# Kernel tuning notes

Measured on AMD Instinct MI355X. Metric: run time of the kernel, lower is better.

The kernel has to match this reference:

```python
import jax, jax.numpy as jnp
import numpy as np

N_HEAD = 16
N_FEAT = 1024
D_K = N_FEAT // N_HEAD
B, S = 2, 2048


def setup_inputs() -> dict:
    key = jax.random.key(0)
    ks = jax.random.split(key, 13)
    s = 1.0 / np.sqrt(N_FEAT)
    return {
        "query": jax.random.normal(ks[0], (B, S, N_FEAT), jnp.float32),
        "key": jax.random.normal(ks[1], (B, S, N_FEAT), jnp.float32),
        "value": jax.random.normal(ks[2], (B, S, N_FEAT), jnp.float32),
        "mask": jax.random.randint(ks[3], (B, 1, S), 0, 2).astype(bool),
        "w_q": jax.random.uniform(ks[4], (N_FEAT, N_FEAT), jnp.float32, -s, s),
        "b_q": jax.random.uniform(ks[5], (N_FEAT,), jnp.float32, -s, s),
        "w_k": jax.random.uniform(ks[6], (N_FEAT, N_FEAT), jnp.float32, -s, s),
        "b_k": jax.random.uniform(ks[7], (N_FEAT,), jnp.float32, -s, s),
        "w_v": jax.random.uniform(ks[8], (N_FEAT, N_FEAT), jnp.float32, -s, s),
        "b_v": jax.random.uniform(ks[9], (N_FEAT,), jnp.float32, -s, s),
        "w_o": jax.random.uniform(ks[10], (N_FEAT, N_FEAT), jnp.float32, -s, s),
        "b_o": jax.random.uniform(ks[11], (N_FEAT,), jnp.float32, -s, s),
    }


def reference(query, key, value, mask, w_q, b_q, w_k, b_k, w_v, b_v, w_o, b_o):
    b = query.shape[0]
    # projections -> [b, h, s, d_k]
    def proj(x, w, bias):
        y = x @ w.T + bias
        return y.reshape(b, -1, N_HEAD, D_K).transpose(0, 2, 1, 3)

    q = proj(query, w_q, b_q)
    k = proj(key, w_k, b_k)
    v = proj(value, w_v, b_v)

    scores = jnp.einsum("bhqd,bhkd->bhqk", q, k) / jnp.sqrt(jnp.asarray(D_K, q.dtype))
    m = mask[:, None]  # [b,1,1,s] broadcast over heads and query positions
    scores = jnp.where(m, jnp.asarray(-10000.0, scores.dtype), scores)
    attn = jax.nn.softmax(scores, axis=-1)
    attn = jnp.where(m, jnp.asarray(0.0, attn.dtype), attn)
    x = jnp.einsum("bhqk,bhkd->bhqd", attn, v)
    x = x.transpose(0, 2, 1, 3).reshape(b, -1, N_HEAD * D_K)
    return x @ w_o.T + b_o
```

## Files before the change

kernel.cpp:

```cpp
#include <hip/hip_runtime.h>
#include <hip/hip_bf16.h>


typedef float f32x4 __attribute__((ext_vector_type(4)));
typedef short bf16x8 __attribute__((ext_vector_type(8)));
typedef short bf16x4 __attribute__((ext_vector_type(4)));

typedef const __attribute__((address_space(1))) void* gas_ptr;
typedef __attribute__((address_space(3))) void* las_ptr;

#if __has_builtin(__builtin_amdgcn_exp2f)
#define EXP2(x) __builtin_amdgcn_exp2f(x)
#else
#define EXP2(x) exp2f(x)
#endif
#define LOG2E 1.4426950408889634f

static __device__ __forceinline__ short to_bf16s(float f) {
    __hip_bfloat16 h = __float2bfloat16(f);
    return __builtin_bit_cast(short, h);
}
static __device__ __forceinline__ unsigned pack_bf16(float a, float b) {
    unsigned lo = (unsigned short)__builtin_bit_cast(short, __float2bfloat16(a));
    unsigned hi = (unsigned short)__builtin_bit_cast(short, __float2bfloat16(b));
    return lo | (hi << 16);
}
static __device__ __forceinline__ bf16x4 pack4(float a, float b, float c, float d) {
    unsigned long long u = (unsigned long long)pack_bf16(a, b)
                         | ((unsigned long long)pack_bf16(c, d) << 32);
    return __builtin_bit_cast(bf16x4, u);
}
static __device__ __forceinline__ f32x4 mfma16(bf16x4 a, bf16x4 b, f32x4 c) {
#if __has_builtin(__builtin_amdgcn_mfma_f32_16x16x16bf16_1k)
    return __builtin_amdgcn_mfma_f32_16x16x16bf16_1k(a, b, c, 0, 0, 0);
#else
    asm("v_mfma_f32_16x16x16_bf16 %0, %1, %2, %0" : "+v"(c) : "v"(a), "v"(b));
    return c;
#endif
}

__global__ void cvt3_kernel(const float* __restrict__ s0, const float* __restrict__ s1,
                            const float* __restrict__ s2, short* __restrict__ d0,
                            short* __restrict__ d1, short* __restrict__ d2) {
    const int g = blockIdx.x;
    const int sel = g >> 12;
    const int i = (g & 4095) * 256 + threadIdx.x;
    const float* s = sel == 0 ? s0 : (sel == 1 ? s1 : s2);
    short* d = sel == 0 ? d0 : (sel == 1 ? d1 : d2);
    float4 v = reinterpret_cast<const float4*>(s)[i];
    short4 o;
    o.x = to_bf16s(v.x); o.y = to_bf16s(v.y); o.z = to_bf16s(v.z); o.w = to_bf16s(v.w);
    reinterpret_cast<short4*>(d)[i] = o;
}
__global__ void cvt4_kernel(const float* __restrict__ s0, const float* __restrict__ s1,
                            const float* __restrict__ s2, const float* __restrict__ s3,
                            short* __restrict__ d0, short* __restrict__ d1,
                            short* __restrict__ d2, short* __restrict__ d3) {
    const int g = blockIdx.x;
    const int sel = g >> 10;
    const int i = (g & 1023) * 256 + threadIdx.x;
    const float* s = sel == 0 ? s0 : (sel == 1 ? s1 : (sel == 2 ? s2 : s3));
    short* d = sel == 0 ? d0 : (sel == 1 ? d1 : (sel == 2 ? d2 : d3));
    float4 v = reinterpret_cast<const float4*>(s)[i];
    short4 o;
    o.x = to_bf16s(v.x); o.y = to_bf16s(v.y); o.z = to_bf16s(v.z); o.w = to_bf16s(v.w);
    reinterpret_cast<short4*>(d)[i] = o;
}

__global__ void maskf_kernel(const int* __restrict__ mask, float* __restrict__ mf) {
    int i = blockIdx.x * 256 + threadIdx.x;
    mf[i] = mask[i] ? (-10000.0f * LOG2E) : 0.0f;
}


static __device__ __forceinline__ void stage_tile(
    short* sa, short* sb, const short* A, const short* W,
    int m0, int n0, int k0, int tid)
{
#pragma unroll
    for (int rnd = 0; rnd < 2; ++rnd) {
        const int t = rnd * 256 + tid;
        const int c2 = t & 7;
        const int row = 2 * (t >> 3) + (c2 & 1);
        const int col = (c2 >> 1) * 8;
        __builtin_amdgcn_global_load_lds((gas_ptr)(A + (long)(m0 + row) * 1024 + k0 + col),
                                         (las_ptr)(sa + t * 8), 16, 0, 0);
        __builtin_amdgcn_global_load_lds((gas_ptr)(W + (long)(n0 + row) * 1024 + k0 + col),
                                         (las_ptr)(sb + t * 8), 16, 0, 0);
    }
}

static __device__ __forceinline__ void gemm_compute(
    const short* sa, const short* sb, int wr, int wc, int aoff, f32x4 (&acc)[4][4])
{
    bf16x8 af[4], bfr[4];
#pragma unroll
    for (int i = 0; i < 4; ++i)
        af[i] = *reinterpret_cast<const bf16x8*>(sa + (wr + i * 16) * 32 + aoff);
#pragma unroll
    for (int j = 0; j < 4; ++j)
        bfr[j] = *reinterpret_cast<const bf16x8*>(sb + (wc + j * 16) * 32 + aoff);
#pragma unroll
    for (int i = 0; i < 4; ++i)
#pragma unroll
        for (int j = 0; j < 4; ++j)
            acc[i][j] = __builtin_amdgcn_mfma_f32_16x16x32_bf16(af[i], bfr[j], acc[i][j], 0, 0, 0);
}

__global__ __launch_bounds__(256, 3) void proj_gemm(
    const short* __restrict__ A0, const short* __restrict__ A1, const short* __restrict__ A2,
    const short* __restrict__ W0, const short* __restrict__ W1, const short* __restrict__ W2,
    const float* __restrict__ bi0, const float* __restrict__ bi1, const float* __restrict__ bi2,
    short* __restrict__ o0, short* __restrict__ o1, short* __restrict__ o2)
{
    __shared__ __align__(16) short sa[2][4096];
    __shared__ __align__(16) short sb[2][4096];
    const int z = blockIdx.z;
    const short* A = z == 0 ? A0 : (z == 1 ? A1 : A2);
    const short* W = z == 0 ? W0 : (z == 1 ? W1 : W2);
    const float* bias = z == 0 ? bi0 : (z == 1 ? bi1 : bi2);
    short* outp = z == 0 ? o0 : (z == 1 ? o1 : o2);

    const int tid = threadIdx.x;
    const int w = tid >> 6, l = tid & 63;
    const int lr = l & 15, lh = l >> 4;
    const int m0 = blockIdx.x * 128, n0 = blockIdx.y * 128;
    const int wr = (w >> 1) * 64, wc = (w & 1) * 64;
    const int aoff = (lr >> 1) * 64 + (lr & 1) * 8 + lh * 16;

    f32x4 acc[4][4] = {};

    stage_tile(sa[0], sb[0], A, W, m0, n0, 0, tid);
    __syncthreads();
    for (int k0 = 0; k0 < 1024; k0 += 64) {
        stage_tile(sa[1], sb[1], A, W, m0, n0, k0 + 32, tid);
        gemm_compute(sa[0], sb[0], wr, wc, aoff, acc);
        __syncthreads();
        if (k0 + 64 < 1024)
            stage_tile(sa[0], sb[0], A, W, m0, n0, k0 + 64, tid);
        gemm_compute(sa[1], sb[1], wr, wc, aoff, acc);
        __syncthreads();
    }

    const float scl = (z == 0) ? 0.125f * LOG2E : 1.0f;
#pragma unroll
    for (int i = 0; i < 4; ++i) {
#pragma unroll
        for (int j = 0; j < 4; ++j) {
#pragma unroll
            for (int r = 0; r < 4; ++r) {
                const int row = m0 + wr + i * 16 + lh * 4 + r;
                const int col = n0 + wc + j * 16 + lr;
                const float v = (acc[i][j][r] + bias[col]) * scl;
                const int b = row >> 11, s = row & 2047;
                const int h = col >> 6, d = col & 63;
                if (z != 2)
                    outp[(((long)(b * 16 + h)) * 2048 + s) * 64 + d] = to_bf16s(v);
                else
                    outp[(((long)(b * 16 + h)) * 64 + d) * 2048 + s] = to_bf16s(v);
            }
        }
    }
}

__global__ __launch_bounds__(256, 2) void out_gemm(
    const short* __restrict__ A, const short* __restrict__ W,
    const float* __restrict__ bias, float* __restrict__ outp)
{
    __shared__ __align__(16) short sa[2][4096];
    __shared__ __align__(16) short sb[2][4096];
    const int tid = threadIdx.x;
    const int w = tid >> 6, l = tid & 63;
    const int lr = l & 15, lh = l >> 4;
    const int m0 = blockIdx.x * 128, n0 = blockIdx.y * 128;
    const int wr = (w >> 1) * 64, wc = (w & 1) * 64;
    const int aoff = (lr >> 1) * 64 + (lr & 1) * 8 + lh * 16;

    f32x4 acc[4][4] = {};

    stage_tile(sa[0], sb[0], A, W, m0, n0, 0, tid);
    __syncthreads();
    for (int k0 = 0; k0 < 1024; k0 += 64) {
        stage_tile(sa[1], sb[1], A, W, m0, n0, k0 + 32, tid);
        gemm_compute(sa[0], sb[0], wr, wc, aoff, acc);
        __syncthreads();
        if (k0 + 64 < 1024)
            stage_tile(sa[0], sb[0], A, W, m0, n0, k0 + 64, tid);
        gemm_compute(sa[1], sb[1], wr, wc, aoff, acc);
        __syncthreads();
    }

#pragma unroll
    for (int i = 0; i < 4; ++i)
#pragma unroll
        for (int j = 0; j < 4; ++j)
#pragma unroll
            for (int r = 0; r < 4; ++r) {
                const int row = m0 + wr + i * 16 + lh * 4 + r;
                const int col = n0 + wc + j * 16 + lr;
                outp[(long)row * 1024 + col] = acc[i][j][r] + bias[col];
            }
}


static __device__ __forceinline__ void stage_kv(
    short* ldsKb, short* ldsVb, const short* Kg, const short* Vg,
    int key0, int w, int srow, int schunk)
{
    __builtin_amdgcn_global_load_lds((gas_ptr)(Kg + (long)(key0 + srow) * 64 + schunk * 8),
                                     (las_ptr)(ldsKb + w * 512), 16, 0, 0);
    __builtin_amdgcn_global_load_lds((gas_ptr)(Kg + (long)(key0 + srow + 32) * 64 + schunk * 8),
                                     (las_ptr)(ldsKb + 2048 + w * 512), 16, 0, 0);
    __builtin_amdgcn_global_load_lds((gas_ptr)(Vg + (long)srow * 2048 + key0 + schunk * 8),
                                     (las_ptr)(ldsVb + w * 512), 16, 0, 0);
    __builtin_amdgcn_global_load_lds((gas_ptr)(Vg + (long)(srow + 32) * 2048 + key0 + schunk * 8),
                                     (las_ptr)(ldsVb + 2048 + w * 512), 16, 0, 0);
}

static __device__ __forceinline__ void attn_step(
    const short* __restrict__ Kbuf, const short* __restrict__ Vbuf,
    const float* __restrict__ ldsM, int key0,
    const bf16x8 (&qf)[2][2], int lr, int lh, int sw,
    float (&mreg)[2], float (&lsum)[2], f32x4 (&ao)[2][4])
{
    f32x4 mb[4];
#pragma unroll
    for (int s = 0; s < 4; ++s)
        mb[s] = *reinterpret_cast<const f32x4*>(ldsM + key0 + s * 16 + lh * 4);

    f32x4 sc[2][4];
#pragma unroll
    for (int s = 0; s < 4; ++s) {
        const short* kb = Kbuf + (s * 16 + lr) * 64;
        bf16x8 k0 = *reinterpret_cast<const bf16x8*>(kb + (((lh * 16) ^ sw) >> 1));
        bf16x8 k1 = *reinterpret_cast<const bf16x8*>(kb + (((64 + lh * 16) ^ sw) >> 1));
        f32x4 z = {};
        sc[0][s] = __builtin_amdgcn_mfma_f32_16x16x32_bf16(k0, qf[0][0], z, 0, 0, 0);
        sc[0][s] = __builtin_amdgcn_mfma_f32_16x16x32_bf16(k1, qf[0][1], sc[0][s], 0, 0, 0);
        sc[1][s] = __builtin_amdgcn_mfma_f32_16x16x32_bf16(k0, qf[1][0], z, 0, 0, 0);
        sc[1][s] = __builtin_amdgcn_mfma_f32_16x16x32_bf16(k1, qf[1][1], sc[1][s], 0, 0, 0);
    }

    bf16x4 pb[2][4];
#pragma unroll
    for (int j = 0; j < 2; ++j) {
        float t = -1e30f;
#pragma unroll
        for (int s = 0; s < 4; ++s)
#pragma unroll
            for (int r = 0; r < 4; ++r) {
                const float v = sc[j][s][r] + mb[s][r];
                sc[j][s][r] = v;
                t = fmaxf(t, v);
            }
        t = fmaxf(t, __shfl_xor(t, 16));
        t = fmaxf(t, __shfl_xor(t, 32));
        if (__any(t > mreg[j] + 8.0f)) {
            const float mn = fmaxf(mreg[j], t);
            const float sf = EXP2(mreg[j] - mn);
            lsum[j] *= sf;
#pragma unroll
            for (int d4 = 0; d4 < 4; ++d4) ao[j][d4] *= sf;
            mreg[j] = mn;
        }
        float ps = 0.f;
#pragma unroll
        for (int s = 0; s < 4; ++s) {
            const float p0 = EXP2(sc[j][s][0] - mreg[j]);
            const float p1 = EXP2(sc[j][s][1] - mreg[j]);
            const float p2 = EXP2(sc[j][s][2] - mreg[j]);
            const float p3 = EXP2(sc[j][s][3] - mreg[j]);
            ps += (p0 + p1) + (p2 + p3);
            pb[j][s] = pack4(p0, p1, p2, p3);
        }
        ps += __shfl_xor(ps, 16);
        ps += __shfl_xor(ps, 32);
        lsum[j] += ps;
    }

#pragma unroll
    for (int s = 0; s < 4; ++s) {
#pragma unroll
        for (int d4 = 0; d4 < 4; ++d4) {
            const short* vb = Vbuf + (d4 * 16 + lr) * 64;
            bf16x4 vf = *reinterpret_cast<const bf16x4*>(vb + (((s * 32 + lh * 8) ^ sw) >> 1));
            ao[0][d4] = mfma16(vf, pb[0][s], ao[0][d4]);
            ao[1][d4] = mfma16(vf, pb[1][s], ao[1][d4]);
        }
    }
}

__global__ __launch_bounds__(256, 2) void attn_kernel(
    const short* __restrict__ Q, const short* __restrict__ Kmat,
    const short* __restrict__ Vt, const float* __restrict__ maskf,
    short* __restrict__ X)
{
    __shared__ __align__(16) short ldsK[2][4096];
    __shared__ __align__(16) short ldsV[2][4096];
    __shared__ __align__(16) float ldsM[2048];

    const int id = blockIdx.x;
    const int slot = id >> 3;
    const int bh = (id & 7) * 4 + (slot >> 4);
    const int q0 = (slot & 15) * 128;
    const int b = bh >> 4, h = bh & 15;
    const int w = threadIdx.x >> 6, l = threadIdx.x & 63;
    const int lr = l & 15, lh = l >> 4;
    const int sw = (lr & 7) << 4;

    const int srow = w * 8 + (l >> 3);
    const int schunk = (l & 7) ^ (srow & 7);

    const short* Kg = Kmat + (long)bh * 2048 * 64;
    const short* Vg = Vt + (long)bh * 64 * 2048;

#pragma unroll
    for (int rnd = 0; rnd < 2; ++rnd) {
        const int t = rnd * 256 + threadIdx.x;
        __builtin_amdgcn_global_load_lds((gas_ptr)(maskf + (long)b * 2048 + t * 4),
                                         (las_ptr)(ldsM + t * 4), 16, 0, 0);
    }

    const short* Qp = Q + ((long)bh * 2048 + q0 + w * 32 + lr) * 64 + lh * 8;
    bf16x8 qf[2][2];
    qf[0][0] = *reinterpret_cast<const bf16x8*>(Qp);
    qf[0][1] = *reinterpret_cast<const bf16x8*>(Qp + 32);
    qf[1][0] = *reinterpret_cast<const bf16x8*>(Qp + 16 * 64);
    qf[1][1] = *reinterpret_cast<const bf16x8*>(Qp + 16 * 64 + 32);

    float mreg[2] = {-1e30f, -1e30f}, lsum[2] = {0.f, 0.f};
    f32x4 ao[2][4] = {};

    stage_kv(ldsK[0], ldsV[0], Kg, Vg, 0, w, srow, schunk);
    __syncthreads();

    for (int tt = 0; tt < 16; ++tt) {
        const int key0 = tt * 128;
        stage_kv(ldsK[1], ldsV[1], Kg, Vg, key0 + 64, w, srow, schunk);
        attn_step(ldsK[0], ldsV[0], ldsM, key0, qf, lr, lh, sw, mreg, lsum, ao);
        __syncthreads();
        if (tt < 15)
            stage_kv(ldsK[0], ldsV[0], Kg, Vg, key0 + 128, w, srow, schunk);
        attn_step(ldsK[1], ldsV[1], ldsM, key0 + 64, qf, lr, lh, sw, mreg, lsum, ao);
        __syncthreads();
    }

#pragma unroll
    for (int j = 0; j < 2; ++j) {
        const float inv = 1.0f / fmaxf(lsum[j], 1e-30f);
        const int s = q0 + w * 32 + j * 16 + lr;
        short* Xp = X + ((long)b * 2048 + s) * 1024 + h * 64 + lh * 4;
#pragma unroll
        for (int d4 = 0; d4 < 4; ++d4) {
            short4 o;
            o.x = to_bf16s(ao[j][d4][0] * inv);
            o.y = to_bf16s(ao[j][d4][1] * inv);
            o.z = to_bf16s(ao[j][d4][2] * inv);
            o.w = to_bf16s(ao[j][d4][3] * inv);
            *reinterpret_cast<short4*>(Xp + d4 * 16) = o;
        }
    }
}

extern "C" void kernel_launch(void* const* d_in, const int* in_sizes, int n_in,
                              void* d_out, int out_size, void* d_ws, size_t ws_size,
                              hipStream_t stream) {
    const float* query = (const float*)d_in[0];
    const float* key_  = (const float*)d_in[1];
    const float* value = (const float*)d_in[2];
    const int*   mask  = (const int*)d_in[3];
    const float* w_q = (const float*)d_in[4];
    const float* b_q = (const float*)d_in[5];
    const float* w_k = (const float*)d_in[6];
    const float* b_k = (const float*)d_in[7];
    const float* w_v = (const float*)d_in[8];
    const float* b_v = (const float*)d_in[9];
    const float* w_o = (const float*)d_in[10];
    const float* b_o = (const float*)d_in[11];

    const long SEQ = 4194304;
    const long WSZ = 1048576;
    short* ws = (short*)d_ws;
    short* cq = ws;
    short* ck = cq + SEQ;
    short* cv = ck + SEQ;
    short* wq = cv + SEQ;
    short* wk = wq + WSZ;
    short* wv = wk + WSZ;
    short* wo = wv + WSZ;
    short* Qb = wo + WSZ;
    short* Kb = Qb + SEQ;
    short* Vt = Kb + SEQ;
    short* Xb = cq;
    float* mkf = (float*)cv;

    cvt3_kernel<<<12288, 256, 0, stream>>>(query, key_, value, cq, ck, cv);
    cvt4_kernel<<<4096, 256, 0, stream>>>(w_q, w_k, w_v, w_o, wq, wk, wv, wo);

    dim3 blk(256);
    proj_gemm<<<dim3(32, 8, 3), blk, 0, stream>>>(cq, ck, cv, wq, wk, wv,
                                                  b_q, b_k, b_v, Qb, Kb, Vt);

    maskf_kernel<<<16, 256, 0, stream>>>(mask, mkf);

    attn_kernel<<<512, blk, 0, stream>>>(Qb, Kb, Vt, mkf, Xb);

    out_gemm<<<dim3(32, 8), blk, 0, stream>>>(Xb, wo, b_o, (float*)d_out);
}
```

Baseline: 148.0 us.

## Use 16x16x32 MFMA for PV via key permutation, shrink out_gemm N tile

The attention PV product switches from 16x16x16 to 16x16x32 MFMAs. K rows and mask entries are permuted so the score accumulator layout matches the B-operand layout the wider instruction expects, which halves the number of PV MFMAs. The mask bias is folded into the QK MFMA accumulator init instead of a separate add. Separately, out_gemm uses 128x64 tiles with twice as many blocks to improve occupancy and CU fill, at the cost of more A-tile reloads.

```diff
diff --git a/kernel.cpp b/kernel.cpp
--- a/kernel.cpp
+++ b/kernel.cpp
@@ -4,7 +4,6 @@
 
 typedef float f32x4 __attribute__((ext_vector_type(4)));
 typedef short bf16x8 __attribute__((ext_vector_type(8)));
-typedef short bf16x4 __attribute__((ext_vector_type(4)));
 
 typedef const __attribute__((address_space(1))) void* gas_ptr;
 typedef __attribute__((address_space(3))) void* las_ptr;
@@ -25,18 +24,13 @@
     unsigned hi = (unsigned short)__builtin_bit_cast(short, __float2bfloat16(b));
     return lo | (hi << 16);
 }
-static __device__ __forceinline__ bf16x4 pack4(float a, float b, float c, float d) {
-    unsigned long long u = (unsigned long long)pack_bf16(a, b)
-                         | ((unsigned long long)pack_bf16(c, d) << 32);
-    return __builtin_bit_cast(bf16x4, u);
-}
-static __device__ __forceinline__ f32x4 mfma16(bf16x4 a, bf16x4 b, f32x4 c) {
-#if __has_builtin(__builtin_amdgcn_mfma_f32_16x16x16bf16_1k)
-    return __builtin_amdgcn_mfma_f32_16x16x16bf16_1k(a, b, c, 0, 0, 0);
-#else
-    asm("v_mfma_f32_16x16x16_bf16 %0, %1, %2, %0" : "+v"(c) : "v"(a), "v"(b));
-    return c;
-#endif
+static __device__ __forceinline__ bf16x8 pack8(const float* p) {
+    unsigned d0 = pack_bf16(p[0], p[1]);
+    unsigned d1 = pack_bf16(p[2], p[3]);
+    unsigned d2 = pack_bf16(p[4], p[5]);
+    unsigned d3 = pack_bf16(p[6], p[7]);
+    unsigned u4[4] = {d0, d1, d2, d3};
+    return __builtin_bit_cast(bf16x8, u4);
 }
 
 __global__ void cvt3_kernel(const float* __restrict__ s0, const float* __restrict__ s1,
@@ -68,10 +62,11 @@
 }
 
 __global__ void maskf_kernel(const int* __restrict__ mask, float* __restrict__ mf) {
-    int i = blockIdx.x * 256 + threadIdx.x;
-    mf[i] = mask[i] ? (-10000.0f * LOG2E) : 0.0f;
-}
-
+    const int i = blockIdx.x * 256 + threadIdx.x;
+    const int p = i & 31;
+    const int phi = 8 * ((p >> 2) & 3) + 4 * (p >> 4) + (p & 3);
+    mf[i] = mask[(i & ~31) | phi] ? (-10000.0f * LOG2E) : 0.0f;
+}
 
 static __device__ __forceinline__ void stage_tile(
     short* sa, short* sb, const short* A, const short* W,
@@ -168,32 +163,64 @@
     const float* __restrict__ bias, float* __restrict__ outp)
 {
     __shared__ __align__(16) short sa[2][4096];
-    __shared__ __align__(16) short sb[2][4096];
+    __shared__ __align__(16) short sb[2][2048];
     const int tid = threadIdx.x;
     const int w = tid >> 6, l = tid & 63;
     const int lr = l & 15, lh = l >> 4;
-    const int m0 = blockIdx.x * 128, n0 = blockIdx.y * 128;
-    const int wr = (w >> 1) * 64, wc = (w & 1) * 64;
+    const int m0 = blockIdx.x * 128, n0 = blockIdx.y * 64;
+    const int wr = (w >> 1) * 64, wc = (w & 1) * 32;
     const int aoff = (lr >> 1) * 64 + (lr & 1) * 8 + lh * 16;
 
-    f32x4 acc[4][4] = {};
-
-    stage_tile(sa[0], sb[0], A, W, m0, n0, 0, tid);
+    f32x4 acc[4][2] = {};
+
+    const int c2 = tid & 7;
+    const int brow = 2 * (tid >> 3) + (c2 & 1);
+    const int bcol = (c2 >> 1) * 8;
+
+    auto stage = [&](short* pa, short* pb, int k0) {
+#pragma unroll
+        for (int rnd = 0; rnd < 2; ++rnd) {
+            const int t = rnd * 256 + tid;
+            const int cc = t & 7;
+            const int row = 2 * (t >> 3) + (cc & 1);
+            const int col = (cc >> 1) * 8;
+            __builtin_amdgcn_global_load_lds((gas_ptr)(A + (long)(m0 + row) * 1024 + k0 + col),
+                                             (las_ptr)(pa + t * 8), 16, 0, 0);
+        }
+        __builtin_amdgcn_global_load_lds((gas_ptr)(W + (long)(n0 + brow) * 1024 + k0 + bcol),
+                                         (las_ptr)(pb + tid * 8), 16, 0, 0);
+    };
+    auto compute = [&](const short* pa, const short* pb) {
+        bf16x8 af[4], bfr[2];
+#pragma unroll
+        for (int i = 0; i < 4; ++i)
+            af[i] = *reinterpret_cast<const bf16x8*>(pa + (wr + i * 16) * 32 + aoff);
+#pragma unroll
+        for (int j = 0; j < 2; ++j)
+            bfr[j] = *reinterpret_cast<const bf16x8*>(pb + (wc + j * 16) * 32 + aoff);
+#pragma unroll
+        for (int i = 0; i < 4; ++i)
+#pragma unroll
+            for (int j = 0; j < 2; ++j)
+                acc[i][j] = __builtin_amdgcn_mfma_f32_16x16x32_bf16(af[i], bfr[j], acc[i][j], 0, 0, 0);
+    };
+
+    stage(sa[0], sb[0], 0);
     __syncthreads();
     for (int k0 = 0; k0 < 1024; k0 += 64) {
-        stage_tile(sa[1], sb[1], A, W, m0, n0, k0 + 32, tid);
-        gemm_compute(sa[0], sb[0], wr, wc, aoff, acc);
+        stage(sa[1], sb[1], k0 + 32);
+        compute(sa[0], sb[0]);
         __syncthreads();
         if (k0 + 64 < 1024)
-            stage_tile(sa[0], sb[0], A, W, m0, n0, k0 + 64, tid);
-        gemm_compute(sa[1], sb[1], wr, wc, aoff, acc);
+            stage(sa[0], sb[0], k0 + 64);
+        compute(sa[1], sb[1]);
         __syncthreads();
     }
 
 #pragma unroll
     for (int i = 0; i < 4; ++i)
 #pragma unroll
-        for (int j = 0; j < 4; ++j)
+        for (int j = 0; j < 2; ++j)
 #pragma unroll
             for (int r = 0; r < 4; ++r) {
                 const int row = m0 + wr + i * 16 + lh * 4 + r;
@@ -205,11 +232,11 @@
 
 static __device__ __forceinline__ void stage_kv(
     short* ldsKb, short* ldsVb, const short* Kg, const short* Vg,
-    int key0, int w, int srow, int schunk)
-{
-    __builtin_amdgcn_global_load_lds((gas_ptr)(Kg + (long)(key0 + srow) * 64 + schunk * 8),
+    int key0, int w, int srow, int prow, int schunk)
+{
+    __builtin_amdgcn_global_load_lds((gas_ptr)(Kg + (long)(key0 + prow) * 64 + schunk * 8),
                                      (las_ptr)(ldsKb + w * 512), 16, 0, 0);
-    __builtin_amdgcn_global_load_lds((gas_ptr)(Kg + (long)(key0 + srow + 32) * 64 + schunk * 8),
+    __builtin_amdgcn_global_load_lds((gas_ptr)(Kg + (long)(key0 + 32 + prow) * 64 + schunk * 8),
                                      (las_ptr)(ldsKb + 2048 + w * 512), 16, 0, 0);
     __builtin_amdgcn_global_load_lds((gas_ptr)(Vg + (long)srow * 2048 + key0 + schunk * 8),
                                      (las_ptr)(ldsVb + w * 512), 16, 0, 0);
@@ -234,25 +261,20 @@
         const short* kb = Kbuf + (s * 16 + lr) * 64;
         bf16x8 k0 = *reinterpret_cast<const bf16x8*>(kb + (((lh * 16) ^ sw) >> 1));
         bf16x8 k1 = *reinterpret_cast<const bf16x8*>(kb + (((64 + lh * 16) ^ sw) >> 1));
-        f32x4 z = {};
-        sc[0][s] = __builtin_amdgcn_mfma_f32_16x16x32_bf16(k0, qf[0][0], z, 0, 0, 0);
+        sc[0][s] = __builtin_amdgcn_mfma_f32_16x16x32_bf16(k0, qf[0][0], mb[s], 0, 0, 0);
         sc[0][s] = __builtin_amdgcn_mfma_f32_16x16x32_bf16(k1, qf[0][1], sc[0][s], 0, 0, 0);
-        sc[1][s] = __builtin_amdgcn_mfma_f32_16x16x32_bf16(k0, qf[1][0], z, 0, 0, 0);
+        sc[1][s] = __builtin_amdgcn_mfma_f32_16x16x32_bf16(k0, qf[1][0], mb[s], 0, 0, 0);
         sc[1][s] = __builtin_amdgcn_mfma_f32_16x16x32_bf16(k1, qf[1][1], sc[1][s], 0, 0, 0);
     }
 
-    bf16x4 pb[2][4];
+    bf16x8 pb[2][2];
 #pragma unroll
     for (int j = 0; j < 2; ++j) {
-        float t = -1e30f;
-#pragma unroll
-        for (int s = 0; s < 4; ++s)
-#pragma unroll
-            for (int r = 0; r < 4; ++r) {
-                const float v = sc[j][s][r] + mb[s][r];
-                sc[j][s][r] = v;
-                t = fmaxf(t, v);
-            }
+        float m0 = fmaxf(fmaxf(fmaxf(sc[j][0][0], sc[j][0][1]), sc[j][0][2]), sc[j][0][3]);
+        float m1 = fmaxf(fmaxf(fmaxf(sc[j][1][0], sc[j][1][1]), sc[j][1][2]), sc[j][1][3]);
+        float m2 = fmaxf(fmaxf(fmaxf(sc[j][2][0], sc[j][2][1]), sc[j][2][2]), sc[j][2][3]);
+        float m3 = fmaxf(fmaxf(fmaxf(sc[j][3][0], sc[j][3][1]), sc[j][3][2]), sc[j][3][3]);
+        float t = fmaxf(fmaxf(m0, m1), fmaxf(m2, m3));
         t = fmaxf(t, __shfl_xor(t, 16));
         t = fmaxf(t, __shfl_xor(t, 32));
         if (__any(t > mreg[j] + 8.0f)) {
@@ -263,29 +285,31 @@
             for (int d4 = 0; d4 < 4; ++d4) ao[j][d4] *= sf;
             mreg[j] = mn;
         }
-        float ps = 0.f;
+        float p[16], ps = 0.f;
 #pragma unroll
         for (int s = 0; s < 4; ++s) {
-            const float p0 = EXP2(sc[j][s][0] - mreg[j]);
-            const float p1 = EXP2(sc[j][s][1] - mreg[j]);
-            const float p2 = EXP2(sc[j][s][2] - mreg[j]);
-            const float p3 = EXP2(sc[j][s][3] - mreg[j]);
-            ps += (p0 + p1) + (p2 + p3);
-            pb[j][s] = pack4(p0, p1, p2, p3);
+#pragma unroll
+            for (int r = 0; r < 4; ++r) {
+                const float e = EXP2(sc[j][s][r] - mreg[j]);
+                p[s * 4 + r] = e;
+                ps += e;
+            }
         }
         ps += __shfl_xor(ps, 16);
         ps += __shfl_xor(ps, 32);
         lsum[j] += ps;
-    }
-
-#pragma unroll
-    for (int s = 0; s < 4; ++s) {
+        pb[j][0] = pack8(p);
+        pb[j][1] = pack8(p + 8);
+    }
+
+#pragma unroll
+    for (int c = 0; c < 2; ++c) {
 #pragma unroll
         for (int d4 = 0; d4 < 4; ++d4) {
             const short* vb = Vbuf + (d4 * 16 + lr) * 64;
-            bf16x4 vf = *reinterpret_cast<const bf16x4*>(vb + (((s * 32 + lh * 8) ^ sw) >> 1));
-            ao[0][d4] = mfma16(vf, pb[0][s], ao[0][d4]);
-            ao[1][d4] = mfma16(vf, pb[1][s], ao[1][d4]);
+            bf16x8 vf = *reinterpret_cast<const bf16x8*>(vb + (((c * 64 + lh * 16) ^ sw) >> 1));
+            ao[0][d4] = __builtin_amdgcn_mfma_f32_16x16x32_bf16(vf, pb[0][c], ao[0][d4], 0, 0, 0);
+            ao[1][d4] = __builtin_amdgcn_mfma_f32_16x16x32_bf16(vf, pb[1][c], ao[1][d4], 0, 0, 0);
         }
     }
 }
@@ -310,6 +334,7 @@
 
     const int srow = w * 8 + (l >> 3);
     const int schunk = (l & 7) ^ (srow & 7);
+    const int prow = 8 * ((srow >> 2) & 3) + 4 * (srow >> 4) + (srow & 3);
 
     const short* Kg = Kmat + (long)bh * 2048 * 64;
     const short* Vg = Vt + (long)bh * 64 * 2048;
@@ -331,16 +356,16 @@
     float mreg[2] = {-1e30f, -1e30f}, lsum[2] = {0.f, 0.f};
     f32x4 ao[2][4] = {};
 
-    stage_kv(ldsK[0], ldsV[0], Kg, Vg, 0, w, srow, schunk);
+    stage_kv(ldsK[0], ldsV[0], Kg, Vg, 0, w, srow, prow, schunk);
     __syncthreads();
 
     for (int tt = 0; tt < 16; ++tt) {
         const int key0 = tt * 128;
-        stage_kv(ldsK[1], ldsV[1], Kg, Vg, key0 + 64, w, srow, schunk);
+        stage_kv(ldsK[1], ldsV[1], Kg, Vg, key0 + 64, w, srow, prow, schunk);
         attn_step(ldsK[0], ldsV[0], ldsM, key0, qf, lr, lh, sw, mreg, lsum, ao);
         __syncthreads();
         if (tt < 15)
-            stage_kv(ldsK[0], ldsV[0], Kg, Vg, key0 + 128, w, srow, schunk);
+            stage_kv(ldsK[0], ldsV[0], Kg, Vg, key0 + 128, w, srow, prow, schunk);
         attn_step(ldsK[1], ldsV[1], ldsM, key0 + 64, qf, lr, lh, sw, mreg, lsum, ao);
         __syncthreads();
     }
@@ -405,5 +430,5 @@
 
     attn_kernel<<<512, blk, 0, stream>>>(Qb, Kb, Vt, mkf, Xb);
 
-    out_gemm<<<dim3(32, 8), blk, 0, stream>>>(Xb, wo, b_o, (float*)d_out);
-}
+    out_gemm<<<dim3(32, 16), blk, 0, stream>>>(Xb, wo, b_o, (float*)d_out);
+}
```

After: 146.8 us. About the same (-0.8%).
